# Kernel optimization log

Measured on AMD Instinct MI355X. Metric: run time of the kernel, lower is better.

## Reference

```python
import jax, jax.numpy as jnp
import numpy as np

N = 500_000   # num nodes
F = 128       # num_features
H = 128       # hidden
B = 32_768    # batch size
K = 4         # hops
RWS = 16      # random walks per batch node
E = RWS * B   # sampled edges per hop
ALPHA = 0.1
OUT = 8


def setup_inputs() -> dict:
    key = jax.random.key(0)
    ks = jax.random.split(key, 12)
    x = jax.random.normal(ks[0], (N, F), dtype=jnp.float32)
    degree = jax.random.uniform(ks[1], (N,), dtype=jnp.float32, minval=1.0, maxval=64.0)
    batch = jax.random.randint(ks[2], (B,), 0, N, dtype=jnp.int32)
    heads_idx = jax.random.randint(ks[3], (K, E), 0, B, dtype=jnp.int32)
    ends = jax.random.randint(ks[4], (K, E), 0, N, dtype=jnp.int32)
    # MLP params (Kaiming-ish scaling)
    W0 = jax.random.normal(ks[5], (F, H), dtype=jnp.float32) / np.float32(np.sqrt(F))
    b0 = jnp.zeros((H,), dtype=jnp.float32)
    W1 = jax.random.normal(ks[6], (H, H), dtype=jnp.float32) / np.float32(np.sqrt(H))
    b1 = jnp.zeros((H,), dtype=jnp.float32)
    W2 = jax.random.normal(ks[7], (H, OUT), dtype=jnp.float32) / np.float32(np.sqrt(H))
    b2 = jnp.zeros((OUT,), dtype=jnp.float32)
    # APPNP attention weights: alpha*(1-alpha)^k, last = (1-alpha)^K
    att = np.float32(ALPHA) * np.float32(1.0 - ALPHA) ** np.arange(K + 1, dtype=np.float32)
    att[-1] = np.float32(1.0 - ALPHA) ** np.float32(K)
    att = jnp.asarray(att)
    return {"x": x, "W0": W0, "b0": b0, "W1": W1, "b1": b1, "W2": W2, "b2": b2,
            "att": att, "degree": degree, "batch": batch,
            "heads_idx": heads_idx, "ends": ends}


def reference(x, W0, b0, W1, b1, W2, b2, att, degree, batch, heads_idx, ends):
    # eval mode: dropout is a no-op
    dis = degree ** -0.5  # deg_inv_sqrt

    def mlp(feats):  # lins[1](relu(lins[0](feats)))
        h = jax.nn.relu(feats @ W0 + b0)
        return h @ W1 + b1

    nb = batch.shape[0]
    ne = jnp.float32(ends.shape[1])
    dsum = degree[batch].sum()

    aggx = att[0] * mlp(x[batch])                       # [B, H]
    for k in range(K):  # small fixed hop count
        heads = heads_idx[k]                            # local rows in [0, B)
        e = ends[k]                                     # global node ids
        val = dis[batch[heads]] * dis[e] * (dsum / ne)  # [E]
        tmp = mlp(x[e]) * val[:, None]                  # gather + MLP + weight
        aggx = aggx + att[k + 1] * jax.ops.segment_sum(tmp, heads, num_segments=nb)
    out = jax.nn.relu(aggx) @ W2 + b2                   # [B, 8]
    return jax.nn.log_softmax(out, axis=1)
```

## Files before the change

### kernel.cpp

```cpp
#include <hip/hip_runtime.h>

#define NN 500000
#define FF 128
#define HH 128
#define BB 32768
#define KHOPS 4
#define EPER 524288
#define KE (KHOPS * EPER)
#define NOUT 8
#define SBLK 256
#define EPB (KE / SBLK)

typedef unsigned short u16;
typedef __attribute__((ext_vector_type(8))) short short8v;
typedef __attribute__((ext_vector_type(4))) float f32x4;

__device__ __forceinline__ float bf2f(u16 v) {
    union { unsigned int u; float f; } t; t.u = ((unsigned int)v) << 16; return t.f;
}
__device__ __forceinline__ float bflo(unsigned int u) {
    union { unsigned int x; float f; } t; t.x = u << 16; return t.f;
}
__device__ __forceinline__ float bfhi(unsigned int u) {
    union { unsigned int x; float f; } t; t.x = u & 0xFFFF0000u; return t.f;
}
__device__ __forceinline__ u16 f2bf(float f) {
    union { float f; unsigned int u; } t; t.f = f;
    unsigned int u = t.u;
    unsigned int r = (u + 0x7FFFu + ((u >> 16) & 1u)) >> 16;
    return (u16)r;
}

__global__ void k_degsum1(const float* __restrict__ deg, const int* __restrict__ batch,
                          float* __restrict__ partial) {
    __shared__ float red[256];
    int i = blockIdx.x * 256 + threadIdx.x;
    red[threadIdx.x] = deg[batch[i]];
    __syncthreads();
    for (int off = 128; off > 0; off >>= 1) {
        if (threadIdx.x < off) red[threadIdx.x] += red[threadIdx.x + off];
        __syncthreads();
    }
    if (threadIdx.x == 0) partial[blockIdx.x] = red[0];
}
__global__ void k_degsum2(const float* __restrict__ partial, float* __restrict__ dsum) {
    __shared__ float red[128];
    red[threadIdx.x] = partial[threadIdx.x];
    __syncthreads();
    for (int off = 64; off > 0; off >>= 1) {
        if (threadIdx.x < off) red[threadIdx.x] += red[threadIdx.x + off];
        __syncthreads();
    }
    if (threadIdx.x == 0) *dsum = red[0];
}

__launch_bounds__(256, 1)
__global__ void k_hist2(const int* __restrict__ heads, u16* __restrict__ M) {
    __shared__ unsigned int hp[16384];
    int tid = threadIdx.x, blk = blockIdx.x;
    #pragma unroll
    for (int j = 0; j < 64; j++) hp[tid + j * 256] = 0;
    __syncthreads();
    int ebase = blk * EPB;
    #pragma unroll 4
    for (int it = 0; it < EPB / 256; it++) {
        int b = heads[ebase + it * 256 + tid];
        atomicAdd(&hp[b >> 1], (b & 1) ? 65536u : 1u);
    }
    __syncthreads();
    unsigned int* M32 = (unsigned int*)M;
    #pragma unroll
    for (int j = 0; j < 64; j++) {
        int w = tid + j * 256;
        M32[(size_t)blk * (BB / 2) + w] = hp[w];
    }
}

__global__ void k_colscan(u16* __restrict__ M, int* __restrict__ colsum) {
    int key = blockIdx.x * 256 + threadIdx.x;
    unsigned int run = 0;
    #pragma unroll 8
    for (int b = 0; b < SBLK; b++) {
        size_t idx = (size_t)b * BB + key;
        u16 v = M[idx];
        M[idx] = (u16)run;
        run += v;
    }
    colsum[key] = (int)run;
}

__global__ void k_scan(const int* __restrict__ colsum, int* __restrict__ base) {
    __shared__ int sc[1024];
    int tid = threadIdx.x;
    int loc[32];
    int run = 0;
    #pragma unroll
    for (int j = 0; j < 32; j++) {
        loc[j] = run;
        run += colsum[tid * 32 + j];
    }
    sc[tid] = run;
    __syncthreads();
    for (int off = 1; off < 1024; off <<= 1) {
        int v = (tid >= off) ? sc[tid - off] : 0;
        __syncthreads();
        sc[tid] += v;
        __syncthreads();
    }
    int excl = sc[tid] - run;
    #pragma unroll
    for (int j = 0; j < 32; j++) base[tid * 32 + j] = excl + loc[j];
    if (tid == 1023) base[BB] = sc[1023];
}

__launch_bounds__(256, 1)
__global__ void k_scatter2(const int* __restrict__ heads, const int* __restrict__ ends,
                           const u16* __restrict__ M, const int* __restrict__ base,
                           unsigned int* __restrict__ pe) {
    __shared__ unsigned int hp[16384];
    int tid = threadIdx.x, blk = blockIdx.x;
    #pragma unroll
    for (int j = 0; j < 64; j++) hp[tid + j * 256] = 0;
    __syncthreads();
    int ebase = blk * EPB;
    for (int it = 0; it < EPB / 256; it++) {
        int i = ebase + it * 256 + tid;
        int b = heads[i];
        unsigned int e = (unsigned int)ends[i];
        unsigned int kk = (unsigned int)(i >> 19);
        unsigned int old = atomicAdd(&hp[b >> 1], (b & 1) ? 65536u : 1u);
        unsigned int rank = (b & 1) ? (old >> 16) : (old & 0xFFFFu);
        int pos = base[b] + (int)M[(size_t)blk * BB + b] + (int)rank;
        pe[pos] = (kk << 19) | e;
    }
}

__global__ void k_packW0(const float* __restrict__ W0, u16* __restrict__ w0p) {
    int f = blockIdx.x * 256 + threadIdx.x;
    int k = f >> 7, c = f & 127;
    int kt = k >> 5, i = k & 7, lh = (k >> 3) & 3;
    int lane = lh * 16 + (c & 15), n = c >> 4;
    w0p[(((kt * 8 + n) * 64 + lane) << 3) + i] = f2bf(W0[f]);
}

__launch_bounds__(256, 2)
__global__ void k_gemm1(const float* __restrict__ x, const u16* __restrict__ w0p,
                        const float* __restrict__ b0, u16* __restrict__ h) {
    __shared__ u16 xs[128 * 128];
    __shared__ u16 ws[128 * 128];
    int tid = threadIdx.x;
    int wid = tid >> 6;
    int lane = tid & 63;
    long rowbase = (long)blockIdx.x * 128;

    #pragma unroll
    for (int r = 0; r < 8; r++) {
        int f = tid + r * 256;
        *(float4*)&ws[f * 8] = *(const float4*)&w0p[f * 8];
    }
    #pragma unroll
    for (int r = 0; r < 16; r++) {
        int f = tid + r * 256;
        int row = f >> 5;
        int c4 = (f & 31) * 4;
        long grow = rowbase + row; if (grow >= NN) grow = NN - 1;
        float4 v = *(const float4*)&x[grow * 128 + c4];
        ushort4 pv;
        pv.x = f2bf(v.x); pv.y = f2bf(v.y); pv.z = f2bf(v.z); pv.w = f2bf(v.w);
        int byte = row * 256 + ((c4 * 2) ^ ((row & 7) << 4));
        *(ushort4*)((char*)xs + byte) = pv;
    }
    __syncthreads();

    short8v a[2][4];
    #pragma unroll
    for (int rs = 0; rs < 2; rs++) {
        int row = wid * 32 + rs * 16 + (lane & 15);
        int sw = (row & 7) << 4;
        #pragma unroll
        for (int kt = 0; kt < 4; kt++) {
            int kb = kt * 64 + (lane >> 4) * 16;
            a[rs][kt] = *(const short8v*)((const char*)xs + row * 256 + (kb ^ sw));
        }
    }

    f32x4 acc[2][8] = {};
    #pragma unroll
    for (int n = 0; n < 8; n++) {
        short8v bfr[4];
        #pragma unroll
        for (int kt = 0; kt < 4; kt++)
            bfr[kt] = *(const short8v*)&ws[(((kt * 8 + n) * 64 + lane) << 3)];
        #pragma unroll
        for (int rs = 0; rs < 2; rs++) {
            #pragma unroll
            for (int kt = 0; kt < 4; kt++)
                acc[rs][n] = __builtin_amdgcn_mfma_f32_16x16x32_bf16(
                                 a[rs][kt], bfr[kt], acc[rs][n], 0, 0, 0);
        }
    }

    float b0v[8];
    #pragma unroll
    for (int n = 0; n < 8; n++) b0v[n] = b0[n * 16 + (lane & 15)];
    #pragma unroll
    for (int rs = 0; rs < 2; rs++) {
        #pragma unroll
        for (int r = 0; r < 4; r++) {
            long grow = rowbase + wid * 32 + rs * 16 + (lane >> 4) * 4 + r;
            if (grow < NN) {
                #pragma unroll
                for (int n = 0; n < 8; n++) {
                    float v = acc[rs][n][r] + b0v[n];
                    v = v > 0.f ? v : 0.f;
                    h[grow * 128 + n * 16 + (lane & 15)] = f2bf(v);
                }
            }
        }
    }
}

__launch_bounds__(256)
__global__ void k_gather(const u16* __restrict__ h, const int* __restrict__ batch,
                         const int* __restrict__ base, const unsigned int* __restrict__ pe,
                         const float* __restrict__ deg, const float* __restrict__ att,
                         const float* __restrict__ dsum,
                         float* __restrict__ P, float* __restrict__ s) {
    int b = blockIdx.x * 4 + (threadIdx.x >> 6);
    int l = threadIdx.x & 63;
    int q = l >> 4;
    int c8 = (l & 15) * 8;
    float att0 = att[0];
    float a1 = att[1], a2 = att[2], a3 = att[3], a4 = att[4];
    float scale = dsum[0] * (1.0f / (float)EPER);
    float disb = rsqrtf(deg[batch[b]]) * scale;
    float acc[8] = {0.f, 0.f, 0.f, 0.f, 0.f, 0.f, 0.f, 0.f};

    if (q == 0) {
        int nb = batch[b];
        uint4 v = *(const uint4*)&h[(size_t)nb * 128 + c8];
        acc[0] = att0 * bflo(v.x); acc[1] = att0 * bfhi(v.x);
        acc[2] = att0 * bflo(v.y); acc[3] = att0 * bfhi(v.y);
        acc[4] = att0 * bflo(v.z); acc[5] = att0 * bfhi(v.z);
        acc[6] = att0 * bflo(v.w); acc[7] = att0 * bfhi(v.w);
    }

    int beg = base[b], fin = base[b + 1];
    float wsum = 0.f;
    #pragma unroll 2
    for (int j = beg; j < fin; j += 4) {
        int je = j + q;
        int jc = je < fin ? je : beg;
        unsigned int p = pe[jc];
        int e = (int)(p & 0x7FFFFu);
        int k = (int)(p >> 19);
        float av = (k < 2) ? (k == 0 ? a1 : a2) : (k == 2 ? a3 : a4);
        float w = av * disb * rsqrtf(deg[e]);
        if (je >= fin) w = 0.f;
        uint4 v = *(const uint4*)&h[(size_t)e * 128 + c8];
        acc[0] += w * bflo(v.x); acc[1] += w * bfhi(v.x);
        acc[2] += w * bflo(v.y); acc[3] += w * bfhi(v.y);
        acc[4] += w * bflo(v.z); acc[5] += w * bfhi(v.z);
        acc[6] += w * bflo(v.w); acc[7] += w * bfhi(v.w);
        wsum += w;
    }
    #pragma unroll
    for (int k = 0; k < 8; k++) {
        acc[k] += __shfl_xor(acc[k], 16);
        acc[k] += __shfl_xor(acc[k], 32);
    }
    wsum += __shfl_xor(wsum, 16);
    wsum += __shfl_xor(wsum, 32);

    if (q == 0) {
        float4 o0 = { acc[0], acc[1], acc[2], acc[3] };
        float4 o1 = { acc[4], acc[5], acc[6], acc[7] };
        *(float4*)&P[(size_t)b * 128 + c8]     = o0;
        *(float4*)&P[(size_t)b * 128 + c8 + 4] = o1;
        if (l == 0) s[b] = att0 + wsum;
    }
}

__launch_bounds__(256, 2)
__global__ void k_out(const float* __restrict__ P, const float* __restrict__ s,
                      const float* __restrict__ W1, const float* __restrict__ b1,
                      const float* __restrict__ W2, const float* __restrict__ b2,
                      float* __restrict__ out) {
    __shared__ float W1s[128 * 128];
    __shared__ float Ps[32 * 128];
    int tid = threadIdx.x;
    int rowbase = blockIdx.x * 32;
    #pragma unroll
    for (int rep = 0; rep < 16; rep++) {
        int f = tid + rep * 256;
        *(float4*)&W1s[f * 4] = *(const float4*)&W1[f * 4];
    }
    #pragma unroll
    for (int rep = 0; rep < 4; rep++) {
        int f = tid + rep * 256;
        *(float4*)&Ps[f * 4] = *(const float4*)&P[(size_t)rowbase * 128 + f * 4];
    }
    __syncthreads();

    int c0 = (tid & 31) * 4;
    int r0 = (tid >> 5) * 4;
    float b1r[4] = { b1[c0], b1[c0 + 1], b1[c0 + 2], b1[c0 + 3] };
    float sv[4];
    #pragma unroll
    for (int j = 0; j < 4; j++) sv[j] = s[rowbase + r0 + j];

    float acc[4][4] = {};
    #pragma unroll 2
    for (int i = 0; i < 128; i += 4) {
        float4 xq[4], wq4[4];
        #pragma unroll
        for (int j = 0; j < 4; j++) xq[j]  = *(const float4*)&Ps[(r0 + j) * 128 + i];
        #pragma unroll
        for (int q = 0; q < 4; q++) wq4[q] = *(const float4*)&W1s[(i + q) * 128 + c0];
        #pragma unroll
        for (int j = 0; j < 4; j++) {
            float xv[4] = { xq[j].x, xq[j].y, xq[j].z, xq[j].w };
            #pragma unroll
            for (int q = 0; q < 4; q++) {
                acc[j][0] += xv[q] * wq4[q].x;
                acc[j][1] += xv[q] * wq4[q].y;
                acc[j][2] += xv[q] * wq4[q].z;
                acc[j][3] += xv[q] * wq4[q].w;
            }
        }
    }
    __syncthreads();
    #pragma unroll
    for (int j = 0; j < 4; j++) {
        #pragma unroll
        for (int c = 0; c < 4; c++) {
            float v = acc[j][c] + sv[j] * b1r[c];
            Ps[(r0 + j) * 128 + c0 + c] = v > 0.f ? v : 0.f;
        }
    }
    __syncthreads();

    int row = tid >> 3;
    int o = tid & 7;
    int rot = (row * 4) & 127;
    float v = b2[o];
    #pragma unroll 4
    for (int ii = 0; ii < 128; ii++) {
        int i = (ii + rot) & 127;
        v += Ps[row * 128 + i] * W2[i * 8 + o];
    }
    float m = v;
    for (int d = 1; d < 8; d <<= 1) m = fmaxf(m, __shfl_xor(m, d, 8));
    float ex = expf(v - m);
    float sum = ex;
    for (int d = 1; d < 8; d <<= 1) sum += __shfl_xor(sum, d, 8);
    out[(size_t)(rowbase + row) * 8 + o] = (v - m) - logf(sum);
}

extern "C" void kernel_launch(void* const* d_in, const int* in_sizes, int n_in,
                              void* d_out, int out_size, void* d_ws, size_t ws_size,
                              hipStream_t stream) {
    const float* x     = (const float*)d_in[0];
    const float* W0    = (const float*)d_in[1];
    const float* b0    = (const float*)d_in[2];
    const float* W1    = (const float*)d_in[3];
    const float* b1    = (const float*)d_in[4];
    const float* W2    = (const float*)d_in[5];
    const float* b2    = (const float*)d_in[6];
    const float* att   = (const float*)d_in[7];
    const float* deg   = (const float*)d_in[8];
    const int*   batch = (const int*)d_in[9];
    const int*   heads = (const int*)d_in[10];
    const int*   ends  = (const int*)d_in[11];
    float* out = (float*)d_out;

    char* w = (char*)d_ws;
    size_t off = 0;
    u16* h = (u16*)(w + off);          off += (size_t)NN * 128 * 2;
    float* P = (float*)(w + off);      off += (size_t)BB * 128 * 4;
    float* s = (float*)(w + off);      off += (size_t)BB * 4;
    int* base = (int*)(w + off);       off += 131328;
    unsigned int* pe = (unsigned int*)(w + off); off += (size_t)KE * 4;
    u16* M = (u16*)(w + off);          off += (size_t)SBLK * BB * 2;
    int* colsum = (int*)(w + off);     off += (size_t)BB * 4;
    float* partial = (float*)(w + off); off += 1024;
    float* dsum = (float*)(w + off);   off += 256;
    u16* w0p = (u16*)(w + off);        off += 16384 * 2;

    k_degsum1<<<128, 256, 0, stream>>>(deg, batch, partial);
    k_degsum2<<<1, 128, 0, stream>>>(partial, dsum);
    k_hist2<<<SBLK, 256, 0, stream>>>(heads, M);
    k_colscan<<<BB / 256, 256, 0, stream>>>(M, colsum);
    k_scan<<<1, 1024, 0, stream>>>(colsum, base);
    k_scatter2<<<SBLK, 256, 0, stream>>>(heads, ends, M, base, pe);
    k_packW0<<<64, 256, 0, stream>>>(W0, w0p);
    k_gemm1<<<(NN + 127) / 128, 256, 0, stream>>>(x, w0p, b0, h);
    k_gather<<<BB / 4, 256, 0, stream>>>(h, batch, base, pe, deg, att, dsum, P, s);
    k_out<<<BB / 32, 256, 0, stream>>>(P, s, W1, b1, W2, b2, out);
}
```

Baseline: 327.5 us.

## Precompute edge weights in scatter, byte histograms, batch gather loads

The scatter pass now computes each edge's full weight (hop attention × dis[batch] × dis[end] × scale) from new precomputed dis/disb arrays. It stores the weight alongside the end id, so the gather no longer does a random deg[e] lookup or rsqrt. The gather loop issues 8 independent index and row loads before accumulating, to raise memory-level parallelism. The histogram switches to 8-bit packed counters with twice as many sort blocks, halving LDS per block to allow two blocks per CU. In exchange the edge array doubles to 8 bytes per entry, and the 8-bit counters assume no per-block or running count per head exceeds 255.

```diff
diff --git a/kernel.cpp b/kernel.cpp
--- a/kernel.cpp
+++ b/kernel.cpp
@@ -8,16 +8,14 @@
 #define EPER 524288
 #define KE (KHOPS * EPER)
 #define NOUT 8
-#define SBLK 256
+#define SBLK 512
 #define EPB (KE / SBLK)
 
 typedef unsigned short u16;
+typedef unsigned char u8;
 typedef __attribute__((ext_vector_type(8))) short short8v;
 typedef __attribute__((ext_vector_type(4))) float f32x4;
 
-__device__ __forceinline__ float bf2f(u16 v) {
-    union { unsigned int u; float f; } t; t.u = ((unsigned int)v) << 16; return t.f;
-}
 __device__ __forceinline__ float bflo(unsigned int u) {
     union { unsigned int x; float f; } t; t.x = u << 16; return t.f;
 }
@@ -54,36 +52,44 @@
     if (threadIdx.x == 0) *dsum = red[0];
 }
 
-__launch_bounds__(256, 1)
-__global__ void k_hist2(const int* __restrict__ heads, u16* __restrict__ M) {
-    __shared__ unsigned int hp[16384];
+__global__ void k_prep(const float* __restrict__ deg, const int* __restrict__ batch,
+                       const float* __restrict__ dsum,
+                       float* __restrict__ dis, float* __restrict__ disb) {
+    int i = blockIdx.x * 256 + threadIdx.x;
+    if (i < NN) dis[i] = rsqrtf(deg[i]);
+    if (i < BB) disb[i] = rsqrtf(deg[batch[i]]) * (dsum[0] * (1.0f / (float)EPER));
+}
+
+__launch_bounds__(256, 2)
+__global__ void k_hist2(const int* __restrict__ heads, u8* __restrict__ M) {
+    __shared__ unsigned int hp[8192];
     int tid = threadIdx.x, blk = blockIdx.x;
     #pragma unroll
-    for (int j = 0; j < 64; j++) hp[tid + j * 256] = 0;
+    for (int j = 0; j < 32; j++) hp[tid + j * 256] = 0;
     __syncthreads();
     int ebase = blk * EPB;
     #pragma unroll 4
     for (int it = 0; it < EPB / 256; it++) {
         int b = heads[ebase + it * 256 + tid];
-        atomicAdd(&hp[b >> 1], (b & 1) ? 65536u : 1u);
-    }
-    __syncthreads();
-    unsigned int* M32 = (unsigned int*)M;
-    #pragma unroll
-    for (int j = 0; j < 64; j++) {
+        atomicAdd(&hp[b >> 2], 1u << ((b & 3) * 8));
+    }
+    __syncthreads();
+    unsigned int* M32 = (unsigned int*)(M + (size_t)blk * BB);
+    #pragma unroll
+    for (int j = 0; j < 32; j++) {
         int w = tid + j * 256;
-        M32[(size_t)blk * (BB / 2) + w] = hp[w];
-    }
-}
-
-__global__ void k_colscan(u16* __restrict__ M, int* __restrict__ colsum) {
+        M32[w] = hp[w];
+    }
+}
+
+__global__ void k_colscan(u8* __restrict__ M, int* __restrict__ colsum) {
     int key = blockIdx.x * 256 + threadIdx.x;
     unsigned int run = 0;
     #pragma unroll 8
     for (int b = 0; b < SBLK; b++) {
         size_t idx = (size_t)b * BB + key;
-        u16 v = M[idx];
-        M[idx] = (u16)run;
+        u8 v = M[idx];
+        M[idx] = (u8)run;
         run += v;
     }
     colsum[key] = (int)run;
@@ -113,25 +119,30 @@
     if (tid == 1023) base[BB] = sc[1023];
 }
 
-__launch_bounds__(256, 1)
+__launch_bounds__(256, 2)
 __global__ void k_scatter2(const int* __restrict__ heads, const int* __restrict__ ends,
-                           const u16* __restrict__ M, const int* __restrict__ base,
-                           unsigned int* __restrict__ pe) {
-    __shared__ unsigned int hp[16384];
+                           const u8* __restrict__ M, const int* __restrict__ base,
+                           const float* __restrict__ dis, const float* __restrict__ disb,
+                           const float* __restrict__ att, uint2* __restrict__ ewp) {
+    __shared__ unsigned int hp[8192];
     int tid = threadIdx.x, blk = blockIdx.x;
-    #pragma unroll
-    for (int j = 0; j < 64; j++) hp[tid + j * 256] = 0;
+    float attk = att[(blk >> 7) + 1];
+    #pragma unroll
+    for (int j = 0; j < 32; j++) hp[tid + j * 256] = 0;
     __syncthreads();
     int ebase = blk * EPB;
     for (int it = 0; it < EPB / 256; it++) {
         int i = ebase + it * 256 + tid;
         int b = heads[i];
-        unsigned int e = (unsigned int)ends[i];
-        unsigned int kk = (unsigned int)(i >> 19);
-        unsigned int old = atomicAdd(&hp[b >> 1], (b & 1) ? 65536u : 1u);
-        unsigned int rank = (b & 1) ? (old >> 16) : (old & 0xFFFFu);
+        int e = ends[i];
+        float w = attk * disb[b] * dis[e];
+        unsigned int old = atomicAdd(&hp[b >> 2], 1u << ((b & 3) * 8));
+        unsigned int rank = (old >> ((b & 3) * 8)) & 0xFFu;
         int pos = base[b] + (int)M[(size_t)blk * BB + b] + (int)rank;
-        pe[pos] = (kk << 19) | e;
+        uint2 pw;
+        pw.x = (unsigned int)e;
+        pw.y = __float_as_uint(w);
+        ewp[pos] = pw;
     }
 }
 
@@ -222,18 +233,14 @@
 
 __launch_bounds__(256)
 __global__ void k_gather(const u16* __restrict__ h, const int* __restrict__ batch,
-                         const int* __restrict__ base, const unsigned int* __restrict__ pe,
-                         const float* __restrict__ deg, const float* __restrict__ att,
-                         const float* __restrict__ dsum,
+                         const int* __restrict__ base, const uint2* __restrict__ ewp,
+                         const float* __restrict__ att,
                          float* __restrict__ P, float* __restrict__ s) {
     int b = blockIdx.x * 4 + (threadIdx.x >> 6);
     int l = threadIdx.x & 63;
     int q = l >> 4;
     int c8 = (l & 15) * 8;
     float att0 = att[0];
-    float a1 = att[1], a2 = att[2], a3 = att[3], a4 = att[4];
-    float scale = dsum[0] * (1.0f / (float)EPER);
-    float disb = rsqrtf(deg[batch[b]]) * scale;
     float acc[8] = {0.f, 0.f, 0.f, 0.f, 0.f, 0.f, 0.f, 0.f};
 
     if (q == 0) {
@@ -247,22 +254,28 @@
 
     int beg = base[b], fin = base[b + 1];
     float wsum = 0.f;
-    #pragma unroll 2
-    for (int j = beg; j < fin; j += 4) {
-        int je = j + q;
-        int jc = je < fin ? je : beg;
-        unsigned int p = pe[jc];
-        int e = (int)(p & 0x7FFFFu);
-        int k = (int)(p >> 19);
-        float av = (k < 2) ? (k == 0 ? a1 : a2) : (k == 2 ? a3 : a4);
-        float w = av * disb * rsqrtf(deg[e]);
-        if (je >= fin) w = 0.f;
-        uint4 v = *(const uint4*)&h[(size_t)e * 128 + c8];
-        acc[0] += w * bflo(v.x); acc[1] += w * bfhi(v.x);
-        acc[2] += w * bflo(v.y); acc[3] += w * bfhi(v.y);
-        acc[4] += w * bflo(v.z); acc[5] += w * bfhi(v.z);
-        acc[6] += w * bflo(v.w); acc[7] += w * bfhi(v.w);
-        wsum += w;
+    for (int j = beg; j < fin; j += 32) {
+        uint2 pw[8];
+        #pragma unroll
+        for (int u = 0; u < 8; u++) {
+            int je = j + u * 4 + q;
+            int jc = je < fin ? je : beg;
+            pw[u] = ewp[jc];
+            if (je >= fin) pw[u].y = 0u;
+        }
+        uint4 v[8];
+        #pragma unroll
+        for (int u = 0; u < 8; u++)
+            v[u] = *(const uint4*)&h[(size_t)pw[u].x * 128 + c8];
+        #pragma unroll
+        for (int u = 0; u < 8; u++) {
+            float w = __uint_as_float(pw[u].y);
+            acc[0] += w * bflo(v[u].x); acc[1] += w * bfhi(v[u].x);
+            acc[2] += w * bflo(v[u].y); acc[3] += w * bfhi(v[u].y);
+            acc[4] += w * bflo(v[u].z); acc[5] += w * bfhi(v[u].z);
+            acc[6] += w * bflo(v[u].w); acc[7] += w * bfhi(v[u].w);
+            wsum += w;
+        }
     }
     #pragma unroll
     for (int k = 0; k < 8; k++) {
@@ -380,21 +393,24 @@
     float* P = (float*)(w + off);      off += (size_t)BB * 128 * 4;
     float* s = (float*)(w + off);      off += (size_t)BB * 4;
     int* base = (int*)(w + off);       off += 131328;
-    unsigned int* pe = (unsigned int*)(w + off); off += (size_t)KE * 4;
-    u16* M = (u16*)(w + off);          off += (size_t)SBLK * BB * 2;
+    uint2* ewp = (uint2*)(w + off);    off += (size_t)KE * 8;
+    u8* M = (u8*)(w + off);            off += (size_t)SBLK * BB;
     int* colsum = (int*)(w + off);     off += (size_t)BB * 4;
+    float* dis = (float*)(w + off);    off += (size_t)NN * 4;
+    float* disb = (float*)(w + off);   off += (size_t)BB * 4;
     float* partial = (float*)(w + off); off += 1024;
     float* dsum = (float*)(w + off);   off += 256;
     u16* w0p = (u16*)(w + off);        off += 16384 * 2;
 
     k_degsum1<<<128, 256, 0, stream>>>(deg, batch, partial);
     k_degsum2<<<1, 128, 0, stream>>>(partial, dsum);
+    k_prep<<<(NN + 255) / 256, 256, 0, stream>>>(deg, batch, dsum, dis, disb);
     k_hist2<<<SBLK, 256, 0, stream>>>(heads, M);
     k_colscan<<<BB / 256, 256, 0, stream>>>(M, colsum);
     k_scan<<<1, 1024, 0, stream>>>(colsum, base);
-    k_scatter2<<<SBLK, 256, 0, stream>>>(heads, ends, M, base, pe);
+    k_scatter2<<<SBLK, 256, 0, stream>>>(heads, ends, M, base, dis, disb, att, ewp);
     k_packW0<<<64, 256, 0, stream>>>(W0, w0p);
     k_gemm1<<<(NN + 127) / 128, 256, 0, stream>>>(x, w0p, b0, h);
-    k_gather<<<BB / 4, 256, 0, stream>>>(h, batch, base, pe, deg, att, dsum, P, s);
+    k_gather<<<BB / 4, 256, 0, stream>>>(h, batch, base, ewp, att, P, s);
     k_out<<<BB / 32, 256, 0, stream>>>(P, s, W1, b1, W2, b2, out);
 }
```

Measured after the change: 336.4 us. 1.03x slower.
